# Performance work log

Measured on AMD Instinct MI355X. Metric: run time of the kernel, lower is better.

The kernel has to match this reference:

```python
import jax, jax.numpy as jnp
import numpy as np

PEAK_THRESH = 0.2
PEAK_WEIGHT = 5.0
FOCAL_GAMMA = 2.0
ALPHA_COUNT, ALPHA_HEATMAP, ALPHA_CONF = 1.0, 10.0, 1.5
EPS = 1e-6


def setup_inputs() -> dict:
    key = jax.random.key(0)
    k1, k2, k3, k4, k5, k6 = jax.random.split(key, 6)
    B, P, K, H, W = 16, 20, 17, 64, 64
    return {
        "count_logits": jax.random.normal(k1, (B, P + 1), dtype=jnp.float32),
        "pred_heatmaps": jax.random.normal(k2, (B, P, K, H, W), dtype=jnp.float32),
        "pred_conf_logits": jax.random.normal(k3, (B, P), dtype=jnp.float32),
        "gt_heatmaps": jax.random.uniform(k4, (B, P, K, H, W), dtype=jnp.float32),
        "count": jax.random.randint(k5, (B,), 0, P + 1, dtype=jnp.int32),
        "mask": jax.random.randint(k6, (B, P), 0, 2, dtype=jnp.int32),
    }


def _cross_entropy(logits, labels):
    logp = jax.nn.log_softmax(logits, axis=-1)
    return -jnp.mean(jnp.take_along_axis(logp, labels[:, None], axis=-1))


def _peak_mse(pred, gt, mask_f):
    # weight map: 1 everywhere, PEAK_WEIGHT where gt > thresh
    w = jnp.where(gt > PEAK_THRESH, PEAK_WEIGHT, 1.0)
    m = mask_f[:, :, None, None, None]  # [B,P,1,1,1]
    diff = (pred - gt) ** 2 * w * m
    B, P, K, H, W = pred.shape
    return diff.sum() / (mask_f.sum() * K * H * W + EPS)


def _focal_loss(logits, targets):
    # stable BCE-with-logits, elementwise
    bce = jnp.maximum(logits, 0.0) - logits * targets + jnp.log1p(jnp.exp(-jnp.abs(logits)))
    p_t = jnp.exp(-bce)
    return jnp.mean((1.0 - p_t) ** FOCAL_GAMMA * bce)


def reference(count_logits, pred_heatmaps, pred_conf_logits, gt_heatmaps, count, mask):
    mask_f = mask.astype(pred_heatmaps.dtype)
    loss_count = _cross_entropy(count_logits, count)
    hm = _peak_mse(pred_heatmaps, gt_heatmaps, mask_f)
    loss_heatmap = jnp.where(mask_f.sum() > 0, hm, 0.0)
    loss_conf = _focal_loss(pred_conf_logits, mask_f)
    total = ALPHA_COUNT * loss_count + ALPHA_HEATMAP * loss_heatmap + ALPHA_CONF * loss_conf
    return total
```

## Files before the change

### kernel.cpp

```cpp
#include <hip/hip_runtime.h>
#include <hip/hip_bf16.h>


#define B_      16
#define P_      20
#define NBP     (B_ * P_)
#define KHW     (17 * 64 * 64)
#define KHW4    (KHW / 4)
#define TOTAL4  (NBP * KHW4)
#define NBLOCKS 4096
#define NTHREADS 256

#define PEAK_THRESH 0.2f
#define PEAK_WEIGHT 5.0f

__global__ __launch_bounds__(NTHREADS)
void hm_partial_kernel(const float4* __restrict__ pred,
                       const float4* __restrict__ gt,
                       const int*    __restrict__ mask,
                       float*        __restrict__ partial) {
    float acc = 0.0f;
    const int stride = gridDim.x * blockDim.x;
    for (int i = blockIdx.x * blockDim.x + threadIdx.x; i < TOTAL4; i += stride) {
        const int slice = i / KHW4;
        if (mask[slice] != 0) {
            const float4 p = pred[i];
            const float4 g = gt[i];
            float d, w;
            d = p.x - g.x; w = (g.x > PEAK_THRESH) ? PEAK_WEIGHT : 1.0f; acc += d * d * w;
            d = p.y - g.y; w = (g.y > PEAK_THRESH) ? PEAK_WEIGHT : 1.0f; acc += d * d * w;
            d = p.z - g.z; w = (g.z > PEAK_THRESH) ? PEAK_WEIGHT : 1.0f; acc += d * d * w;
            d = p.w - g.w; w = (g.w > PEAK_THRESH) ? PEAK_WEIGHT : 1.0f; acc += d * d * w;
        }
    }
    #pragma unroll
    for (int off = 32; off > 0; off >>= 1) acc += __shfl_down(acc, off);

    __shared__ float s[NTHREADS / 64];
    if ((threadIdx.x & 63) == 0) s[threadIdx.x >> 6] = acc;
    __syncthreads();
    if (threadIdx.x == 0) {
        float t = 0.0f;
        #pragma unroll
        for (int w = 0; w < NTHREADS / 64; ++w) t += s[w];
        partial[blockIdx.x] = t;
    }
}

__global__ __launch_bounds__(64)
void finalize_kernel(const float* __restrict__ partial,
                     const float* __restrict__ count_logits,
                     const int*   __restrict__ count,
                     const float* __restrict__ conf_logits,
                     const int*   __restrict__ mask,
                     float*       __restrict__ out) {
    const int lane = threadIdx.x;

    float ds = 0.0f;
    for (int i = lane; i < NBLOCKS; i += 64) ds += partial[i];

    float ms = 0.0f, fs = 0.0f;
    for (int i = lane; i < NBP; i += 64) {
        const float t = (float)mask[i];
        ms += t;
        const float l   = conf_logits[i];
        const float bce = fmaxf(l, 0.0f) - l * t + log1pf(expf(-fabsf(l)));
        const float pt  = expf(-bce);
        const float om  = 1.0f - pt;
        fs += om * om * bce;
    }

    float ce = 0.0f;
    if (lane < B_) {
        const float* row = count_logits + lane * (P_ + 1);
        float mx = row[0];
        #pragma unroll
        for (int j = 1; j < P_ + 1; ++j) mx = fmaxf(mx, row[j]);
        float se = 0.0f;
        #pragma unroll
        for (int j = 0; j < P_ + 1; ++j) se += expf(row[j] - mx);
        const float lse = mx + logf(se);
        ce = -(row[count[lane]] - lse);
    }

    #pragma unroll
    for (int off = 32; off > 0; off >>= 1) {
        ds += __shfl_down(ds, off);
        ms += __shfl_down(ms, off);
        fs += __shfl_down(fs, off);
        ce += __shfl_down(ce, off);
    }

    if (lane == 0) {
        const float loss_count = ce / (float)B_;
        const float loss_conf  = fs / (float)NBP;
        const float hm         = ds / (ms * (float)KHW + 1e-6f);
        const float loss_hm    = (ms > 0.0f) ? hm : 0.0f;
        out[0] = 1.0f * loss_count + 10.0f * loss_hm + 1.5f * loss_conf;
    }
}

extern "C" void kernel_launch(void* const* d_in, const int* in_sizes, int n_in,
                              void* d_out, int out_size, void* d_ws, size_t ws_size,
                              hipStream_t stream) {
    const float* count_logits = (const float*)d_in[0];
    const float* pred_hm      = (const float*)d_in[1];
    const float* conf_logits  = (const float*)d_in[2];
    const float* gt_hm        = (const float*)d_in[3];
    const int*   count        = (const int*)d_in[4];
    const int*   mask         = (const int*)d_in[5];
    float*       out          = (float*)d_out;
    float*       partial      = (float*)d_ws;

    hm_partial_kernel<<<NBLOCKS, NTHREADS, 0, stream>>>(
        (const float4*)pred_hm, (const float4*)gt_hm, mask, partial);

    finalize_kernel<<<1, 64, 0, stream>>>(
        partial, count_logits, count, conf_logits, mask, out);
}
```

Baseline: 203.2 us.

## Compact active mask slices and stride only over active heatmap work

Each block builds a compacted list of active (mask != 0) slices in shared memory using a wave ballot, then iterates only over elements of those slices instead of checking the mask per element across the full tensor. Each thread now processes two float4 pairs per iteration and the grid is halved. This targets wasted iterations and load imbalance from masked-out slices, at the cost of redundant per-block compaction work and an integer divide per iteration.

```diff
diff --git a/kernel.cpp b/kernel.cpp
--- a/kernel.cpp
+++ b/kernel.cpp
@@ -1,5 +1,4 @@
 #include <hip/hip_runtime.h>
-#include <hip/hip_bf16.h>
 
 
 #define B_      16
@@ -7,32 +6,60 @@
 #define NBP     (B_ * P_)
 #define KHW     (17 * 64 * 64)
 #define KHW4    (KHW / 4)
-#define TOTAL4  (NBP * KHW4)
-#define NBLOCKS 4096
+#define KHW8    (KHW / 8)
+#define NBLOCKS 2048
 #define NTHREADS 256
 
 #define PEAK_THRESH 0.2f
 #define PEAK_WEIGHT 5.0f
+
+__device__ __forceinline__ float wdiff4(const float4 p, const float4 g) {
+    float d, w, a;
+    d = p.x - g.x; w = (g.x > PEAK_THRESH) ? PEAK_WEIGHT : 1.0f; a  = d * d * w;
+    d = p.y - g.y; w = (g.y > PEAK_THRESH) ? PEAK_WEIGHT : 1.0f; a += d * d * w;
+    d = p.z - g.z; w = (g.z > PEAK_THRESH) ? PEAK_WEIGHT : 1.0f; a += d * d * w;
+    d = p.w - g.w; w = (g.w > PEAK_THRESH) ? PEAK_WEIGHT : 1.0f; a += d * d * w;
+    return a;
+}
 
 __global__ __launch_bounds__(NTHREADS)
 void hm_partial_kernel(const float4* __restrict__ pred,
                        const float4* __restrict__ gt,
                        const int*    __restrict__ mask,
                        float*        __restrict__ partial) {
+    __shared__ int s_act[NBP];
+    __shared__ int s_cnt;
+    const int lane = threadIdx.x & 63;
+    if (threadIdx.x < 64) {
+        int base = 0;
+        #pragma unroll
+        for (int r = 0; r < NBP / 64; ++r) {
+            const int idx = r * 64 + lane;
+            const bool m = (mask[idx] != 0);
+            const unsigned long long bal = __ballot(m);
+            if (m) {
+                const int pos = __popcll(bal & ((1ull << lane) - 1ull));
+                s_act[base + pos] = idx;
+            }
+            base += __popcll(bal);
+        }
+        if (lane == 0) s_cnt = base;
+    }
+    __syncthreads();
+
+    const int total = s_cnt * KHW8;
+    const int stride = gridDim.x * blockDim.x;
     float acc = 0.0f;
-    const int stride = gridDim.x * blockDim.x;
-    for (int i = blockIdx.x * blockDim.x + threadIdx.x; i < TOTAL4; i += stride) {
-        const int slice = i / KHW4;
-        if (mask[slice] != 0) {
-            const float4 p = pred[i];
-            const float4 g = gt[i];
-            float d, w;
-            d = p.x - g.x; w = (g.x > PEAK_THRESH) ? PEAK_WEIGHT : 1.0f; acc += d * d * w;
-            d = p.y - g.y; w = (g.y > PEAK_THRESH) ? PEAK_WEIGHT : 1.0f; acc += d * d * w;
-            d = p.z - g.z; w = (g.z > PEAK_THRESH) ? PEAK_WEIGHT : 1.0f; acc += d * d * w;
-            d = p.w - g.w; w = (g.w > PEAK_THRESH) ? PEAK_WEIGHT : 1.0f; acc += d * d * w;
-        }
+    for (int j = blockIdx.x * blockDim.x + threadIdx.x; j < total; j += stride) {
+        const int slice = j / KHW8;
+        const int off   = j - slice * KHW8;
+        const int b4    = (s_act[slice] * KHW8 + off) * 2;
+        const float4 p0 = pred[b4], p1 = pred[b4 + 1];
+        const float4 g0 = gt[b4],   g1 = gt[b4 + 1];
+        acc += wdiff4(p0, g0);
+        acc += wdiff4(p1, g1);
     }
+
     #pragma unroll
     for (int off = 32; off > 0; off >>= 1) acc += __shfl_down(acc, off);
 
```

Measured after the change: 194.6 us. 4.2% less time.
